# Kernel optimization log

Hardware: AMD Instinct MI355X
Metric: run time of the kernel (lower is better)

## Reference

```python
import jax, jax.numpy as jnp
from jax import lax
import numpy as np

K_IN, K_OUT, H, ML = 32, 16, 256, 80
L_PRE, L_FWD, B = 60, 80, 1024


def gru_cell(x, h, Wih, Whh, bih, bhh):
    # torch GRU gate order: r, z, n
    gi = x @ Wih.T + bih
    gh = h @ Whh.T + bhh
    ir, iz, inn = jnp.split(gi, 3, axis=-1)
    hr, hz, hn = jnp.split(gh, 3, axis=-1)
    r = jax.nn.sigmoid(ir + hr)
    z = jax.nn.sigmoid(iz + hz)
    n = jnp.tanh(inn + r * hn)
    return (1.0 - z) * n + z * h


def setup_inputs() -> dict:
    key = jax.random.key(0)
    ks = jax.random.split(key, 24)
    s = 0.05
    rn = lambda k, shp: (jax.random.normal(k, shp) * s).astype(jnp.float32)
    inp = {
        "pre_x": jax.random.normal(ks[0], (L_PRE, B, K_IN), dtype=jnp.float32),
        "pre_y": jax.random.normal(ks[1], (L_PRE, B, K_OUT), dtype=jnp.float32),
        "forward_x": jax.random.normal(ks[2], (L_FWD, B, K_IN), dtype=jnp.float32),
        # encoder: embedding Linear(k_in+k_out -> H), GRU(H,H)
        "enc_emb_W": rn(ks[3], (H, K_IN + K_OUT)),
        "enc_emb_b": rn(ks[4], (H,)),
        "enc_Wih": rn(ks[5], (3 * H, H)),
        "enc_Whh": rn(ks[6], (3 * H, H)),
        "enc_bih": rn(ks[7], (3 * H,)),
        "enc_bhh": rn(ks[8], (3 * H,)),
        # decoder: embedding Linear(k_out+k_in -> H), attn Linear(2H -> ML),
        # attn_combine Linear(2H -> H), GRU(H,H), out Linear(H -> k_out)
        "dec_emb_W": rn(ks[9], (H, K_OUT + K_IN)),
        "dec_emb_b": rn(ks[10], (H,)),
        "attn_W": rn(ks[11], (ML, 2 * H)),
        "attn_b": rn(ks[12], (ML,)),
        "comb_W": rn(ks[13], (H, 2 * H)),
        "comb_b": rn(ks[14], (H,)),
        "dec_Wih": rn(ks[15], (3 * H, H)),
        "dec_Whh": rn(ks[16], (3 * H, H)),
        "dec_bih": rn(ks[17], (3 * H,)),
        "dec_bhh": rn(ks[18], (3 * H,)),
        "out_W": rn(ks[19], (K_OUT, H)),
        "out_b": rn(ks[20], (K_OUT,)),
    }
    return inp


def reference(pre_x, pre_y, forward_x,
              enc_emb_W, enc_emb_b, enc_Wih, enc_Whh, enc_bih, enc_bhh,
              dec_emb_W, dec_emb_b, attn_W, attn_b, comb_W, comb_b,
              dec_Wih, dec_Whh, dec_bih, dec_bhh, out_W, out_b):
    L_pre, batch, _ = pre_x.shape
    hdim = enc_emb_b.shape[0]
    max_len = attn_b.shape[0]

    # ---- encoder ----
    emb = jnp.concatenate([pre_x, pre_y], axis=2) @ enc_emb_W.T + enc_emb_b  # [L_pre,B,H]
    h0 = jnp.zeros((batch, hdim), dtype=pre_x.dtype)

    def enc_step(h, x):
        h2 = gru_cell(x, h, enc_Wih, enc_Whh, enc_bih, enc_bhh)
        return h2, h2

    enc_h, enc_outs = lax.scan(enc_step, h0, emb)
    # pad encoder outputs to max_length along time (zeros beyond L_pre)
    enc_outputs = jnp.zeros((max_len, batch, hdim), dtype=pre_x.dtype).at[:L_pre].set(enc_outs)
    enc_bmh = enc_outputs.transpose(1, 0, 2)  # [B, ML, H]

    # ---- decoder (dropout inactive: eval mode) ----
    def dec_step(carry, fx):
        y, h = carry
        di = jnp.concatenate([y, fx], axis=-1)            # [B, k_out+k_in]
        e = di @ dec_emb_W.T + dec_emb_b                   # [B, H]
        logits = jnp.concatenate([e, h], axis=-1) @ attn_W.T + attn_b  # [B, ML]
        aw = jax.nn.softmax(logits, axis=-1)
        ctx = jnp.einsum('bm,bmh->bh', aw, enc_bmh)        # [B, H]
        g = jnp.tanh(jnp.concatenate([e, ctx], axis=-1) @ comb_W.T + comb_b)
        h2 = gru_cell(g, h, dec_Wih, dec_Whh, dec_bih, dec_bhh)
        y2 = h2 @ out_W.T + out_b                          # [B, k_out]
        return (y2, h2), y2

    y_init = jnp.zeros_like(pre_y[0])
    _, ys = lax.scan(dec_step, (y_init, enc_h), forward_x)
    return ys  # [L_fwd, B, k_out]
```

## Files before the change

kernel.cpp:

```cpp
#include <hip/hip_runtime.h>
#include <hip/hip_bf16.h>

#define BATCH 1024
#define HD 256
#define MLEN 80
#define LPRE 60
#define LFWD 80
#define KIN 32
#define KOUT 16

typedef unsigned short bf16_t;
typedef __attribute__((ext_vector_type(8))) short bf16x8;
typedef __attribute__((ext_vector_type(4))) float f32x4;
typedef __attribute__((ext_vector_type(4))) unsigned u32x4;

#define MFMA __builtin_amdgcn_mfma_f32_16x16x32_bf16

__device__ __forceinline__ float bf2f(bf16_t v){ return __uint_as_float(((unsigned)v)<<16); }
__device__ __forceinline__ bf16_t f2bf(float f){
    unsigned u = __float_as_uint(f);
    return (bf16_t)((u + 0x7FFFu + ((u>>16)&1u)) >> 16);
}
__device__ __forceinline__ unsigned pack2(float lo, float hi){
    return (unsigned)f2bf(lo) | ((unsigned)f2bf(hi)<<16);
}
__device__ __forceinline__ float bflo(unsigned d){ return __uint_as_float(d<<16); }
__device__ __forceinline__ float bfhi(unsigned d){ return __uint_as_float(d & 0xffff0000u); }
__device__ __forceinline__ float sigm(float x){ return 1.0f/(1.0f+__expf(-x)); }

#define OFF_Z  262144
#define OFF_IN 524288
#define OFF_HN 655360

__global__ void pack_gru(const float* __restrict__ Wih, const float* __restrict__ Whh,
                         bf16_t* __restrict__ dst)
{
    int T = blockIdx.x*256 + threadIdx.x;
    int grp, local;
    if (T < 16384){ grp=0; local=T; }
    else if (T < 32768){ grp=1; local=T-16384; }
    else if (T < 40960){ grp=2; local=T-32768; }
    else { grp=3; local=T-40960; }
    int nkt = (grp<2)?16:8;
    int nt  = local / (nkt*64);
    int rem = local - nt*(nkt*64);
    int kt  = rem >> 6;
    int l   = rem & 63;
    int n   = nt*16 + (l&15);
    int k0  = kt*32 + ((l>>4)<<3);
    unsigned w[4];
    #pragma unroll
    for (int h2=0; h2<4; h2++){
        float v[2];
        #pragma unroll
        for (int s=0; s<2; s++){
            int k = k0 + h2*2 + s;
            if (grp==0)      v[s] = (k<256)? Wih[(size_t)n*HD + k]       : Whh[(size_t)n*HD + (k-256)];
            else if (grp==1) v[s] = (k<256)? Wih[(size_t)(256+n)*HD + k] : Whh[(size_t)(256+n)*HD + (k-256)];
            else if (grp==2) v[s] = Wih[(size_t)(512+n)*HD + k];
            else             v[s] = Whh[(size_t)(512+n)*HD + k];
        }
        w[h2] = pack2(v[0], v[1]);
    }
    uint4 u = {w[0],w[1],w[2],w[3]};
    *(uint4*)((char*)dst + (size_t)T*16) = u;
}

__global__ void pack_B512(const float* __restrict__ W, bf16_t* __restrict__ dst)
{
    int T = blockIdx.x*256 + threadIdx.x;
    int nt = T >> 10, kt = (T>>6)&15, l = T&63;
    int n = nt*16 + (l&15);
    int k0 = kt*32 + ((l>>4)<<3);
    unsigned w[4];
    #pragma unroll
    for (int h2=0; h2<4; h2++)
        w[h2] = pack2(W[(size_t)n*512 + k0+h2*2], W[(size_t)n*512 + k0+h2*2+1]);
    uint4 u = {w[0],w[1],w[2],w[3]};
    *(uint4*)((char*)dst + (size_t)T*16) = u;
}

__global__ void wfuse_kernel(const float* __restrict__ dembW, const float* __restrict__ dembB,
                             const float* __restrict__ outW, const float* __restrict__ outB,
                             float* __restrict__ Wfuse, float* __restrict__ ebias)
{
    int T = blockIdx.x*256 + threadIdx.x;
    if (T < 65536){
        int k = T >> 8, n = T & 255;
        float acc = 0.f;
        #pragma unroll
        for (int o=0;o<16;o++) acc += dembW[(size_t)n*48 + o]*outW[(size_t)o*HD + k];
        Wfuse[(size_t)k*HD + n] = acc;
    } else if (T < 65792){
        int n = T - 65536;
        float acc = dembB[n];
        #pragma unroll
        for (int o=0;o<16;o++) acc += outB[o]*dembW[(size_t)n*48 + o];
        ebias[n] = acc;
    }
}

__global__ void pack_e(const float* __restrict__ Wfuse, const float* __restrict__ dembW,
                       bf16_t* __restrict__ dst)
{
    int T = blockIdx.x*256 + threadIdx.x;
    int nt = T/576, rem = T - nt*576;
    int kt = rem >> 6, l = rem & 63;
    int n = nt*16 + (l&15);
    int k0 = kt*32 + ((l>>4)<<3);
    unsigned w[4];
    #pragma unroll
    for (int h2=0; h2<4; h2++){
        float v[2];
        #pragma unroll
        for (int s=0;s<2;s++){
            int k = k0 + h2*2 + s;
            v[s] = (kt<8)? Wfuse[(size_t)k*HD + n] : dembW[(size_t)n*48 + 16 + (k-256)];
        }
        w[h2] = pack2(v[0], v[1]);
    }
    uint4 u = {w[0],w[1],w[2],w[3]};
    *(uint4*)((char*)dst + (size_t)T*16) = u;
}

__global__ void pack_logits(const float* __restrict__ Wfuse, const float* __restrict__ dembW,
                            const float* __restrict__ attW, const float* __restrict__ attB,
                            const float* __restrict__ dembB, const float* __restrict__ ebias,
                            bf16_t* __restrict__ BL, bf16_t* __restrict__ BL0,
                            float* __restrict__ lb, float* __restrict__ lb0)
{
    int T = blockIdx.x*256 + threadIdx.x;
    if (T < 5760){
        int variant = (T < 2880) ? 0 : 1;
        int local = variant ? (T-2880) : T;
        int nt = local/576, rem = local - nt*576;
        int kt = rem >> 6, l = rem & 63;
        int m  = nt*16 + (l&15);
        int k0 = kt*32 + ((l>>4)<<3);
        unsigned w[4];
        #pragma unroll
        for (int h2=0; h2<4; h2++){
            float v[2];
            for (int s=0;s<2;s++){
                int k = k0 + h2*2 + s;
                float acc;
                if (kt < 8){
                    if (variant == 0){
                        acc = attW[(size_t)m*512 + 256 + k];
                        for (int n=0;n<256;n++) acc += Wfuse[(size_t)k*HD + n]*attW[(size_t)m*512 + n];
                    } else {
                        acc = attW[(size_t)m*512 + 256 + k];
                    }
                } else {
                    int kp = k - 256;
                    acc = 0.f;
                    for (int n=0;n<256;n++) acc += dembW[(size_t)n*48 + 16 + kp]*attW[(size_t)m*512 + n];
                }
                v[s] = acc;
            }
            w[h2] = pack2(v[0], v[1]);
        }
        uint4 u = {w[0],w[1],w[2],w[3]};
        bf16_t* d = variant ? BL0 : BL;
        *(uint4*)((char*)d + (size_t)local*16) = u;
    } else if (T < 5840){
        int m = T - 5760;
        float acc = attB[m];
        for (int n=0;n<256;n++) acc += ebias[n]*attW[(size_t)m*512 + n];
        lb[m] = acc;
    } else if (T < 5920){
        int m = T - 5840;
        float acc = attB[m];
        for (int n=0;n<256;n++) acc += dembB[n]*attW[(size_t)m*512 + n];
        lb0[m] = acc;
    }
}

__global__ void pack_out(const float* __restrict__ outW, bf16_t* __restrict__ dst)
{
    int T = blockIdx.x*256 + threadIdx.x;
    int kt = T >> 6, l = T & 63;
    int n  = l & 15;
    int k0 = kt*32 + ((l>>4)<<3);
    unsigned w[4];
    #pragma unroll
    for (int h2=0; h2<4; h2++)
        w[h2] = pack2(outW[(size_t)n*HD + k0+h2*2], outW[(size_t)n*HD + k0+h2*2+1]);
    uint4 u = {w[0],w[1],w[2],w[3]};
    *(uint4*)((char*)dst + (size_t)T*16) = u;
}

__global__ __launch_bounds__(256) void emb_kernel(
    const float* __restrict__ px, const float* __restrict__ py,
    const float* __restrict__ embW, const float* __restrict__ embB,
    bf16_t* __restrict__ emb)
{
    __shared__ float Ws[256*49];
    __shared__ float xy[16][48];
    __shared__ float bs[256];
    int t = blockIdx.y, b0 = blockIdx.x*16, tid = threadIdx.x;
    for (int i = tid; i < 256*48; i += 256){ int n=i/48, k=i-n*48; Ws[n*49+k]=embW[i]; }
    bs[tid] = embB[tid];
    for (int i = tid; i < 16*48; i += 256){
        int r=i/48, k=i-r*48;
        xy[r][k] = (k<KIN)? px[((size_t)t*BATCH + b0+r)*KIN + k]
                          : py[((size_t)t*BATCH + b0+r)*KOUT + (k-KIN)];
    }
    __syncthreads();
    int n = tid;
    const float* w = &Ws[n*49];
    for (int r=0;r<16;r++){
        float acc = bs[n];
        #pragma unroll
        for (int k=0;k<48;k++) acc += xy[r][k]*w[k];
        emb[((size_t)t*BATCH + b0+r)*HD + n] = f2bf(acc);
    }
}

__global__ void fxconv(const float* __restrict__ fx, bf16_t* __restrict__ dst)
{
    size_t i = (size_t)blockIdx.x*256 + threadIdx.x;
    const float4* s = (const float4*)(fx + i*8);
    float4 a = s[0], b = s[1];
    uint4 u = { pack2(a.x,a.y), pack2(a.z,a.w), pack2(b.x,b.y), pack2(b.z,b.w) };
    *(uint4*)(dst + i*8) = u;
}

__global__ __launch_bounds__(512) void gru_step2(
    const bf16_t* __restrict__ A0, const bf16_t* __restrict__ A1,
    const bf16_t* __restrict__ Bp,
    const float* __restrict__ bih, const float* __restrict__ bhh,
    const float* __restrict__ hprev, float* __restrict__ hnext,
    bf16_t* __restrict__ hnext_bf, bf16_t* __restrict__ extra_bf)
{
    __shared__ __align__(16) bf16_t As[16][520];
    __shared__ __align__(16) f32x4 redR[4][64];
    __shared__ __align__(16) f32x4 redZ[4][64];
    __shared__ __align__(16) f32x4 redI[4][64];
    int tid = threadIdx.x, b0 = blockIdx.x*16;
    for (int i = tid; i < 1024; i += 512){
        int r = i>>6, c = i&63;
        const bf16_t* src = (c<32)? (A0 + (size_t)(b0+r)*HD + c*8)
                                  : (A1 + (size_t)(b0+r)*HD + (c-32)*8);
        *(uint4*)&As[r][c*8] = *(const uint4*)src;
    }
    __syncthreads();
    int lane = tid & 63, wave = tid >> 6;
    int pairId = wave >> 1, half = wave & 1;
    int jt = blockIdx.y*4 + pairId;
    const char* arow = (const char*)&As[lane&15][(lane>>4)*8];
    const char* bpc = (const char*)Bp;
    size_t loff = (size_t)lane*16;
    size_t offX = half ? (size_t)OFF_HN : (size_t)OFF_IN;
    int kt0 = half*8;
    f32x4 cr={0,0,0,0}, cz={0,0,0,0}, cx={0,0,0,0};
    #pragma unroll
    for (int k8=0; k8<8; k8++){
        int kt = kt0 + k8;
        bf16x8 a  = *(const bf16x8*)(arow + kt*64);
        bf16x8 br = *(const bf16x8*)(bpc + (size_t)(((jt<<4)+kt)<<10) + loff);
        bf16x8 bz = *(const bf16x8*)(bpc + OFF_Z + (size_t)(((jt<<4)+kt)<<10) + loff);
        bf16x8 bx = *(const bf16x8*)(bpc + offX + (size_t)(((jt<<3)+k8)<<10) + loff);
        cr = MFMA(a, br, cr, 0,0,0);
        cz = MFMA(a, bz, cz, 0,0,0);
        cx = MFMA(a, bx, cx, 0,0,0);
    }
    if (half == 0){
        redR[pairId][lane] = cr;
        redZ[pairId][lane] = cz;
        redI[pairId][lane] = cx;
    }
    __syncthreads();
    if (half == 1){
        f32x4 crA = redR[pairId][lane];
        f32x4 czA = redZ[pairId][lane];
        f32x4 ci  = redI[pairId][lane];
        int j = (jt<<4) + (lane&15);
        float b_r = bih[j] + bhh[j];
        float b_z = bih[256+j] + bhh[256+j];
        float b_i = bih[512+j], b_h = bhh[512+j];
        #pragma unroll
        for (int q=0;q<4;q++){
            int b = b0 + ((lane>>4)<<2) + q;
            float rv = sigm(cr[q] + crA[q] + b_r);
            float zv = sigm(cz[q] + czA[q] + b_z);
            float nv = tanhf(ci[q] + b_i + rv*(cx[q] + b_h));
            float h2 = (1.0f - zv)*nv + zv*hprev[(size_t)b*HD + j];
            hnext[(size_t)b*HD + j] = h2;
            bf16_t hb = f2bf(h2);
            hnext_bf[(size_t)b*HD + j] = hb;
            extra_bf[(size_t)b*HD + j] = hb;
        }
    }
}

__global__ __launch_bounds__(1024) void dec_front(
    const bf16_t* __restrict__ hbf, const bf16_t* __restrict__ fxt,
    const bf16_t* __restrict__ enc_out,
    const bf16_t* __restrict__ Be, const bf16_t* __restrict__ BL,
    const bf16_t* __restrict__ Bcmb, const bf16_t* __restrict__ Bout,
    const float* __restrict__ ebp, const float* __restrict__ lbp,
    const float* __restrict__ combB, const float* __restrict__ outB,
    int t, bf16_t* __restrict__ g_out, float* __restrict__ out)
{
    __shared__ __align__(16) bf16_t As[16][296];
    __shared__ __align__(16) bf16_t Eb[16][264];
    __shared__ __align__(16) bf16_t Cb[16][264];
    __shared__ float awL[16][84];
    __shared__ float Cpart[16][256];

    int tid = threadIdx.x, b0 = blockIdx.x*16;

    if (tid < 576){
        int r = tid/36, c = tid - r*36;
        const bf16_t* src = (c<32)? (hbf + (size_t)(b0+r)*HD + c*8)
                                  : (fxt + (size_t)(b0+r)*KIN + (c-32)*8);
        *(uint4*)&As[r][c*8] = *(const uint4*)src;
    }

    int half = tid >> 9;
    int u    = tid & 511;
    int cr_  = u >> 5;
    int cc0  = (u & 31) * 8;
    const bf16_t* cbp = enc_out + ((size_t)(half*30)*BATCH + (b0+cr_))*HD + cc0;
    u32x4 pf[10];
    #pragma unroll
    for (int i=0;i<10;i++) pf[i] = *(const u32x4*)(cbp + (size_t)i*BATCH*HD);

    __syncthreads();

    int lane = tid & 63, wave = tid >> 6;
    const bf16_t* arow = &As[lane&15][(lane>>4)*8];
    size_t loff = (size_t)lane*16;
    int ke0 = t ? 0 : 8;

    {
        f32x4 c = {0,0,0,0};
        for (int kt = ke0; kt < 9; kt++){
            bf16x8 a = *(const bf16x8*)(arow + kt*32);
            bf16x8 b = *(const bf16x8*)((const char*)Be + (size_t)((wave*9+kt)<<10) + loff);
            c = MFMA(a, b, c, 0,0,0);
        }
        int n = (wave<<4) + (lane&15);
        float bbn = ebp[n];
        #pragma unroll
        for (int q=0;q<4;q++) Eb[((lane>>4)<<2)+q][n] = f2bf(c[q] + bbn);
    }
    if (wave < 5){
        f32x4 c = {0,0,0,0};
        #pragma unroll
        for (int kt = 0; kt < 9; kt++){
            bf16x8 a = *(const bf16x8*)(arow + kt*32);
            bf16x8 b = *(const bf16x8*)((const char*)BL + (size_t)((wave*9+kt)<<10) + loff);
            c = MFMA(a, b, c, 0,0,0);
        }
        int m = (wave<<4) + (lane&15);
        float bbm = lbp[m];
        #pragma unroll
        for (int q=0;q<4;q++) awL[((lane>>4)<<2)+q][m] = c[q] + bbm;
    } else if (wave == 5 && t > 0){
        f32x4 c = {0,0,0,0};
        #pragma unroll
        for (int kt = 0; kt < 8; kt++){
            bf16x8 a = *(const bf16x8*)(arow + kt*32);
            bf16x8 b = *(const bf16x8*)((const char*)Bout + (size_t)(kt<<10) + loff);
            c = MFMA(a, b, c, 0,0,0);
        }
        int o = lane & 15;
        float bo = outB[o];
        #pragma unroll
        for (int q=0;q<4;q++){
            int r = ((lane>>4)<<2) + q;
            out[((size_t)(t-1)*BATCH + b0+r)*KOUT + o] = c[q] + bo;
        }
    }
    __syncthreads();

    if (tid < 256){
        int r2 = tid >> 4, l2 = tid & 15;
        float vmax = -1e30f;
        for (int m=l2; m<80; m+=16) vmax = fmaxf(vmax, awL[r2][m]);
        #pragma unroll
        for (int k=1; k<16; k<<=1) vmax = fmaxf(vmax, __shfl_xor(vmax, k, 16));
        float ps = 0.f;
        for (int m=l2; m<80; m+=16){ float v = __expf(awL[r2][m]-vmax); awL[r2][m]=v; ps += v; }
        #pragma unroll
        for (int k=1; k<16; k<<=1) ps += __shfl_xor(ps, k, 16);
        float inv = 1.0f/ps;
        for (int m=l2; m<80; m+=16) awL[r2][m] *= inv;
    }
    __syncthreads();

    float acc[8];
    #pragma unroll
    for (int i=0;i<8;i++) acc[i] = 0.f;
    {
        const float* awr = &awL[cr_][half*30];
        #pragma unroll
        for (int i=0;i<10;i++){
            float w = awr[i];
            acc[0] = fmaf(w, bflo(pf[i][0]), acc[0]);
            acc[1] = fmaf(w, bfhi(pf[i][0]), acc[1]);
            acc[2] = fmaf(w, bflo(pf[i][1]), acc[2]);
            acc[3] = fmaf(w, bfhi(pf[i][1]), acc[3]);
            acc[4] = fmaf(w, bflo(pf[i][2]), acc[4]);
            acc[5] = fmaf(w, bfhi(pf[i][2]), acc[5]);
            acc[6] = fmaf(w, bflo(pf[i][3]), acc[6]);
            acc[7] = fmaf(w, bfhi(pf[i][3]), acc[7]);
        }
        #pragma unroll 5
        for (int i=10;i<30;i++){
            u32x4 v = *(const u32x4*)(cbp + (size_t)i*BATCH*HD);
            float w = awr[i];
            acc[0] = fmaf(w, bflo(v[0]), acc[0]);
            acc[1] = fmaf(w, bfhi(v[0]), acc[1]);
            acc[2] = fmaf(w, bflo(v[1]), acc[2]);
            acc[3] = fmaf(w, bfhi(v[1]), acc[3]);
            acc[4] = fmaf(w, bflo(v[2]), acc[4]);
            acc[5] = fmaf(w, bfhi(v[2]), acc[5]);
            acc[6] = fmaf(w, bflo(v[3]), acc[6]);
            acc[7] = fmaf(w, bfhi(v[3]), acc[7]);
        }
    }
    if (half == 0){
        float4 p0 = {acc[0],acc[1],acc[2],acc[3]};
        float4 p1 = {acc[4],acc[5],acc[6],acc[7]};
        *(float4*)&Cpart[cr_][cc0]   = p0;
        *(float4*)&Cpart[cr_][cc0+4] = p1;
    }
    __syncthreads();

    if (half == 1){
        float4 p0 = *(const float4*)&Cpart[cr_][cc0];
        float4 p1 = *(const float4*)&Cpart[cr_][cc0+4];
        uint4 ov;
        ov.x = pack2(acc[0]+p0.x, acc[1]+p0.y);
        ov.y = pack2(acc[2]+p0.z, acc[3]+p0.w);
        ov.z = pack2(acc[4]+p1.x, acc[5]+p1.y);
        ov.w = pack2(acc[6]+p1.z, acc[7]+p1.w);
        *(uint4*)&Cb[cr_][cc0] = ov;
    }
    __syncthreads();

    {
        const bf16_t* ae = &Eb[lane&15][(lane>>4)*8];
        const bf16_t* ac = &Cb[lane&15][(lane>>4)*8];
        f32x4 c = {0,0,0,0};
        #pragma unroll
        for (int kt=0; kt<16; kt++){
            bf16x8 a = (kt<8)? *(const bf16x8*)(ae + kt*32)
                             : *(const bf16x8*)(ac + (kt-8)*32);
            bf16x8 b = *(const bf16x8*)((const char*)Bcmb + (size_t)(((wave<<4)+kt)<<10) + loff);
            c = MFMA(a, b, c, 0,0,0);
        }
        int n = (wave<<4) + (lane&15);
        float bbn = combB[n];
        #pragma unroll
        for (int q=0;q<4;q++){
            int r = ((lane>>4)<<2) + q;
            g_out[(size_t)(b0+r)*HD + n] = f2bf(tanhf(c[q] + bbn));
        }
    }
}

__global__ __launch_bounds__(256) void final79(
    const float* __restrict__ hf, const float* __restrict__ outW,
    const float* __restrict__ outB, float* __restrict__ ys)
{
    __shared__ float hs[16][260];
    __shared__ float ow[16*260];
    int tid = threadIdx.x, b0 = blockIdx.x*16;
    for (int i=tid;i<4096;i+=256){ int o2=i>>8,k=i&255; ow[o2*260+k]=outW[(size_t)o2*HD+k]; }
    for (int i=tid;i<4096;i+=256){ int r=i>>8,k=i&255; hs[r][k]=hf[(size_t)(b0+r)*HD+k]; }
    __syncthreads();
    int r=tid>>4, o=tid&15;
    float acc=outB[o];
    const float* w=&ow[o*260];
    for(int k=0;k<256;k++) acc += hs[r][k]*w[k];
    ys[((size_t)79*BATCH + b0+r)*KOUT + o] = acc;
}

extern "C" void kernel_launch(void* const* d_in, const int* in_sizes, int n_in,
                              void* d_out, int out_size, void* d_ws, size_t ws_size,
                              hipStream_t stream) {
    const float* pre_x    = (const float*)d_in[0];
    const float* pre_y    = (const float*)d_in[1];
    const float* fwd_x    = (const float*)d_in[2];
    const float* enc_embW = (const float*)d_in[3];
    const float* enc_embB = (const float*)d_in[4];
    const float* enc_Wih  = (const float*)d_in[5];
    const float* enc_Whh  = (const float*)d_in[6];
    const float* enc_bih  = (const float*)d_in[7];
    const float* enc_bhh  = (const float*)d_in[8];
    const float* dec_embW = (const float*)d_in[9];
    const float* dec_embB = (const float*)d_in[10];
    const float* attn_W   = (const float*)d_in[11];
    const float* attn_b   = (const float*)d_in[12];
    const float* comb_W   = (const float*)d_in[13];
    const float* comb_b   = (const float*)d_in[14];
    const float* dec_Wih  = (const float*)d_in[15];
    const float* dec_Whh  = (const float*)d_in[16];
    const float* dec_bih  = (const float*)d_in[17];
    const float* dec_bhh  = (const float*)d_in[18];
    const float* out_W    = (const float*)d_in[19];
    const float* out_b    = (const float*)d_in[20];
    float* out = (float*)d_out;

    char* ws = (char*)d_ws;
    size_t o = 0;
    auto alloc = [&](size_t bytes)->char*{
        char* p = ws + o; o = (o + bytes + 255) & ~(size_t)255; return p;
    };
    bf16_t* EMB     = (bf16_t*)alloc((size_t)LPRE*BATCH*HD*2);
    bf16_t* ENC_OUT = (bf16_t*)alloc((size_t)LPRE*BATCH*HD*2);
    bf16_t* FXB     = (bf16_t*)alloc((size_t)LFWD*BATCH*KIN*2);
    float*  HF0     = (float*) alloc((size_t)BATCH*HD*4);
    float*  HF1     = (float*) alloc((size_t)BATCH*HD*4);
    bf16_t* HB0     = (bf16_t*)alloc((size_t)BATCH*HD*2);
    bf16_t* HB1     = (bf16_t*)alloc((size_t)BATCH*HD*2);
    bf16_t* GBUF    = (bf16_t*)alloc((size_t)BATCH*HD*2);
    bf16_t* DUMMY   = (bf16_t*)alloc((size_t)BATCH*HD*2);
    float*  WFUSE   = (float*) alloc((size_t)256*256*4);
    float*  EBIAS   = (float*) alloc(256*4);
    float*  LB      = (float*) alloc(80*4);
    float*  LB0     = (float*) alloc(80*4);
    bf16_t* PACK_ENC = (bf16_t*)alloc(786432);
    bf16_t* PACK_DEC = (bf16_t*)alloc(786432);
    bf16_t* PACK_CMB = (bf16_t*)alloc(262144);
    bf16_t* PACK_E   = (bf16_t*)alloc(147456);
    bf16_t* PACK_BL  = (bf16_t*)alloc(46080);
    bf16_t* PACK_BL0 = (bf16_t*)alloc(46080);
    bf16_t* PACK_OUT = (bf16_t*)alloc(8192);

    hipMemsetAsync(HF0, 0, (size_t)BATCH*HD*4, stream);
    hipMemsetAsync(HB0, 0, (size_t)BATCH*HD*2, stream);

    dim3 blk(256);
    emb_kernel<<<dim3(64,60), blk, 0, stream>>>(pre_x, pre_y, enc_embW, enc_embB, EMB);
    fxconv<<<dim3(1280), blk, 0, stream>>>(fwd_x, FXB);
    pack_gru<<<dim3(192), blk, 0, stream>>>(enc_Wih, enc_Whh, PACK_ENC);
    pack_gru<<<dim3(192), blk, 0, stream>>>(dec_Wih, dec_Whh, PACK_DEC);
    pack_B512<<<dim3(64), blk, 0, stream>>>(comb_W, PACK_CMB);
    wfuse_kernel<<<dim3(257), blk, 0, stream>>>(dec_embW, dec_embB, out_W, out_b, WFUSE, EBIAS);
    pack_e<<<dim3(36), blk, 0, stream>>>(WFUSE, dec_embW, PACK_E);
    pack_logits<<<dim3(24), blk, 0, stream>>>(WFUSE, dec_embW, attn_W, attn_b, dec_embB,
                                              EBIAS, PACK_BL, PACK_BL0, LB, LB0);
    pack_out<<<dim3(2), blk, 0, stream>>>(out_W, PACK_OUT);

    float*  HF[2] = {HF0, HF1};
    bf16_t* HB[2] = {HB0, HB1};
    int p = 0;

    for (int t = 0; t < LPRE; t++){
        gru_step2<<<dim3(64,4), dim3(512), 0, stream>>>(
            EMB + (size_t)t*BATCH*HD, HB[p], PACK_ENC, enc_bih, enc_bhh,
            HF[p], HF[p^1], HB[p^1], ENC_OUT + (size_t)t*BATCH*HD);
        p ^= 1;
    }
    for (int t = 0; t < LFWD; t++){
        const bf16_t* fxt = FXB + (size_t)t*BATCH*KIN;
        dec_front<<<dim3(64), dim3(1024), 0, stream>>>(
            HB[p], fxt, ENC_OUT,
            PACK_E, t ? PACK_BL : PACK_BL0, PACK_CMB, PACK_OUT,
            t ? EBIAS : dec_embB, t ? LB : LB0, comb_b, out_b,
            t, GBUF, out);
        gru_step2<<<dim3(64,4), dim3(512), 0, stream>>>(
            GBUF, HB[p], PACK_DEC, dec_bih, dec_bhh,
            HF[p], HF[p^1], HB[p^1], DUMMY);
        p ^= 1;
    }
    final79<<<dim3(64), blk, 0, stream>>>(HF[p], out_W, out_b, out);
}
```

Before: 2.462 ms.

## Fold combine weights into embedding and precompute encoder-side combine projection

Precomputes P = enc_out @ comb_W[:,256:]^T once after the encoder, so the context term of attn_combine becomes a weighted sum of projected rows. It also folds the decoder embedding weights into comb_W, so g comes from one GEMM on [h, fx] plus the attention-weighted P. The decoder front is split into an attention/softmax kernel and a 4-way column-parallel combine kernel, giving 256 blocks instead of 64 for the combine step. The cost is an extra kernel launch per step, the attention weights round-tripping through global memory, and extra bf16 rounding in P.

```diff
diff --git a/kernel.cpp b/kernel.cpp
--- a/kernel.cpp
+++ b/kernel.cpp
@@ -98,29 +98,6 @@
         for (int o=0;o<16;o++) acc += outB[o]*dembW[(size_t)n*48 + o];
         ebias[n] = acc;
     }
-}
-
-__global__ void pack_e(const float* __restrict__ Wfuse, const float* __restrict__ dembW,
-                       bf16_t* __restrict__ dst)
-{
-    int T = blockIdx.x*256 + threadIdx.x;
-    int nt = T/576, rem = T - nt*576;
-    int kt = rem >> 6, l = rem & 63;
-    int n = nt*16 + (l&15);
-    int k0 = kt*32 + ((l>>4)<<3);
-    unsigned w[4];
-    #pragma unroll
-    for (int h2=0; h2<4; h2++){
-        float v[2];
-        #pragma unroll
-        for (int s=0;s<2;s++){
-            int k = k0 + h2*2 + s;
-            v[s] = (kt<8)? Wfuse[(size_t)k*HD + n] : dembW[(size_t)n*48 + 16 + (k-256)];
-        }
-        w[h2] = pack2(v[0], v[1]);
-    }
-    uint4 u = {w[0],w[1],w[2],w[3]};
-    *(uint4*)((char*)dst + (size_t)T*16) = u;
 }
 
 __global__ void pack_logits(const float* __restrict__ Wfuse, const float* __restrict__ dembW,
@@ -176,6 +153,48 @@
     }
 }
 
+__global__ void pack_gfold(const float* __restrict__ Wfuse, const float* __restrict__ dembW,
+                           const float* __restrict__ combW, const float* __restrict__ combB,
+                           const float* __restrict__ ebias, const float* __restrict__ dembB,
+                           bf16_t* __restrict__ dst, float* __restrict__ cbf, float* __restrict__ cbf0)
+{
+    int T = blockIdx.x*256 + threadIdx.x;
+    if (T < 9216){
+        int nt = T/576, rem = T - nt*576;
+        int kt = rem >> 6, l = rem & 63;
+        int n = nt*16 + (l&15);
+        int k0 = kt*32 + ((l>>4)<<3);
+        unsigned w[4];
+        for (int h2=0; h2<4; h2++){
+            float v[2];
+            for (int s=0;s<2;s++){
+                int k = k0 + h2*2 + s;
+                float acc = 0.f;
+                if (k < 256){
+                    for (int j=0;j<256;j++) acc += Wfuse[(size_t)k*HD + j]*combW[(size_t)n*512 + j];
+                } else {
+                    int kp = k - 256;
+                    for (int j=0;j<256;j++) acc += dembW[(size_t)j*48 + 16 + kp]*combW[(size_t)n*512 + j];
+                }
+                v[s] = acc;
+            }
+            w[h2] = pack2(v[0], v[1]);
+        }
+        uint4 u = {w[0],w[1],w[2],w[3]};
+        *(uint4*)((char*)dst + (size_t)T*16) = u;
+    } else if (T < 9472){
+        int n = T - 9216;
+        float acc = combB[n];
+        for (int j=0;j<256;j++) acc += ebias[j]*combW[(size_t)n*512 + j];
+        cbf[n] = acc;
+    } else if (T < 9728){
+        int n = T - 9472;
+        float acc = combB[n];
+        for (int j=0;j<256;j++) acc += dembB[j]*combW[(size_t)n*512 + j];
+        cbf0[n] = acc;
+    }
+}
+
 __global__ void pack_out(const float* __restrict__ outW, bf16_t* __restrict__ dst)
 {
     int T = blockIdx.x*256 + threadIdx.x;
@@ -226,6 +245,44 @@
     *(uint4*)(dst + i*8) = u;
 }
 
+__global__ __launch_bounds__(256) void pgemm(
+    const bf16_t* __restrict__ enc, const bf16_t* __restrict__ Bcmb,
+    bf16_t* __restrict__ P)
+{
+    __shared__ __align__(16) bf16_t As[16][264];
+    __shared__ __align__(16) bf16_t Gs[16][264];
+    int tid = threadIdx.x, b0 = blockIdx.x*16, t = blockIdx.y;
+    const bf16_t* src = enc + ((size_t)t*BATCH + b0)*HD;
+    for (int i = tid; i < 512; i += 256){
+        int r = i>>5, c = i&31;
+        *(uint4*)&As[r][c*8] = *(const uint4*)(src + (size_t)r*HD + c*8);
+    }
+    __syncthreads();
+    int lane = tid&63, wave = tid>>6;
+    const bf16_t* arow = &As[lane&15][(lane>>4)*8];
+    size_t loff = (size_t)lane*16;
+    #pragma unroll
+    for (int u=0; u<4; u++){
+        int nt = wave*4 + u;
+        f32x4 c = {0,0,0,0};
+        #pragma unroll
+        for (int k8=0; k8<8; k8++){
+            bf16x8 a = *(const bf16x8*)(arow + k8*32);
+            bf16x8 b = *(const bf16x8*)((const char*)Bcmb + (size_t)(((nt<<4)+8+k8)<<10) + loff);
+            c = MFMA(a, b, c, 0,0,0);
+        }
+        int n = (nt<<4) + (lane&15);
+        #pragma unroll
+        for (int q=0;q<4;q++) Gs[((lane>>4)<<2)+q][n] = f2bf(c[q]);
+    }
+    __syncthreads();
+    bf16_t* dst = P + ((size_t)t*BATCH + b0)*HD;
+    for (int i = tid; i < 512; i += 256){
+        int r = i>>5, c = i&31;
+        *(uint4*)(dst + (size_t)r*HD + c*8) = *(const uint4*)&Gs[r][c*8];
+    }
+}
+
 __global__ __launch_bounds__(512) void gru_step2(
     const bf16_t* __restrict__ A0, const bf16_t* __restrict__ A1,
     const bf16_t* __restrict__ Bp,
@@ -294,58 +351,25 @@
     }
 }
 
-__global__ __launch_bounds__(1024) void dec_front(
+__global__ __launch_bounds__(512) void dec_attn(
     const bf16_t* __restrict__ hbf, const bf16_t* __restrict__ fxt,
-    const bf16_t* __restrict__ enc_out,
-    const bf16_t* __restrict__ Be, const bf16_t* __restrict__ BL,
-    const bf16_t* __restrict__ Bcmb, const bf16_t* __restrict__ Bout,
-    const float* __restrict__ ebp, const float* __restrict__ lbp,
-    const float* __restrict__ combB, const float* __restrict__ outB,
-    int t, bf16_t* __restrict__ g_out, float* __restrict__ out)
+    const bf16_t* __restrict__ BL, const bf16_t* __restrict__ Bout,
+    const float* __restrict__ lbp, const float* __restrict__ outB,
+    int t, float* __restrict__ aw, float* __restrict__ out)
 {
     __shared__ __align__(16) bf16_t As[16][296];
-    __shared__ __align__(16) bf16_t Eb[16][264];
-    __shared__ __align__(16) bf16_t Cb[16][264];
     __shared__ float awL[16][84];
-    __shared__ float Cpart[16][256];
-
     int tid = threadIdx.x, b0 = blockIdx.x*16;
-
-    if (tid < 576){
-        int r = tid/36, c = tid - r*36;
+    for (int i = tid; i < 576; i += 512){
+        int r = i/36, c = i - r*36;
         const bf16_t* src = (c<32)? (hbf + (size_t)(b0+r)*HD + c*8)
                                   : (fxt + (size_t)(b0+r)*KIN + (c-32)*8);
         *(uint4*)&As[r][c*8] = *(const uint4*)src;
     }
-
-    int half = tid >> 9;
-    int u    = tid & 511;
-    int cr_  = u >> 5;
-    int cc0  = (u & 31) * 8;
-    const bf16_t* cbp = enc_out + ((size_t)(half*30)*BATCH + (b0+cr_))*HD + cc0;
-    u32x4 pf[10];
-    #pragma unroll
-    for (int i=0;i<10;i++) pf[i] = *(const u32x4*)(cbp + (size_t)i*BATCH*HD);
-
-    __syncthreads();
-
+    __syncthreads();
     int lane = tid & 63, wave = tid >> 6;
     const bf16_t* arow = &As[lane&15][(lane>>4)*8];
     size_t loff = (size_t)lane*16;
-    int ke0 = t ? 0 : 8;
-
-    {
-        f32x4 c = {0,0,0,0};
-        for (int kt = ke0; kt < 9; kt++){
-            bf16x8 a = *(const bf16x8*)(arow + kt*32);
-            bf16x8 b = *(const bf16x8*)((const char*)Be + (size_t)((wave*9+kt)<<10) + loff);
-            c = MFMA(a, b, c, 0,0,0);
-        }
-        int n = (wave<<4) + (lane&15);
-        float bbn = ebp[n];
-        #pragma unroll
-        for (int q=0;q<4;q++) Eb[((lane>>4)<<2)+q][n] = f2bf(c[q] + bbn);
-    }
     if (wave < 5){
         f32x4 c = {0,0,0,0};
         #pragma unroll
@@ -375,7 +399,6 @@
         }
     }
     __syncthreads();
-
     if (tid < 256){
         int r2 = tid >> 4, l2 = tid & 15;
         float vmax = -1e30f;
@@ -387,79 +410,99 @@
         #pragma unroll
         for (int k=1; k<16; k<<=1) ps += __shfl_xor(ps, k, 16);
         float inv = 1.0f/ps;
-        for (int m=l2; m<80; m+=16) awL[r2][m] *= inv;
-    }
-    __syncthreads();
+        for (int m=l2; m<80; m+=16) aw[(size_t)(b0+r2)*80 + m] = awL[r2][m]*inv;
+    }
+}
+
+__global__ __launch_bounds__(256) void dec_gcomb(
+    const bf16_t* __restrict__ hbf, const bf16_t* __restrict__ fxt,
+    const float* __restrict__ aw, const bf16_t* __restrict__ P,
+    const bf16_t* __restrict__ Bgf, const float* __restrict__ cbf,
+    int kt0, bf16_t* __restrict__ g_out)
+{
+    __shared__ __align__(16) bf16_t As[16][296];
+    __shared__ float aws[16][80];
+    __shared__ float pre[16][68];
+    __shared__ float part[2][16][64];
+    int tid = threadIdx.x, b0 = blockIdx.x*16, y = blockIdx.y;
+
+    int half = tid >> 7;
+    int u = tid & 127;
+    int r_ = u >> 3;
+    int c8 = u & 7;
+    const bf16_t* pbp = P + ((size_t)(half*30)*BATCH + (b0+r_))*HD + y*64 + c8*8;
+    u32x4 pf[15];
+    #pragma unroll
+    for (int i=0;i<15;i++) pf[i] = *(const u32x4*)(pbp + (size_t)i*BATCH*HD);
+
+    for (int i = tid; i < 576; i += 256){
+        int r = i/36, c = i - r*36;
+        const bf16_t* src = (c<32)? (hbf + (size_t)(b0+r)*HD + c*8)
+                                  : (fxt + (size_t)(b0+r)*KIN + (c-32)*8);
+        *(uint4*)&As[r][c*8] = *(const uint4*)src;
+    }
+    for (int i = tid; i < 1280; i += 256){
+        int r = i/80, m = i - r*80;
+        aws[r][m] = aw[(size_t)(b0+r)*80 + m];
+    }
+    __syncthreads();
+
+    int lane = tid & 63, wave = tid >> 6;
+    {
+        const bf16_t* arow = &As[lane&15][(lane>>4)*8];
+        size_t loff = (size_t)lane*16;
+        int nt = y*4 + wave;
+        f32x4 c = {0,0,0,0};
+        for (int kt=kt0; kt<9; kt++){
+            bf16x8 a = *(const bf16x8*)(arow + kt*32);
+            bf16x8 b = *(const bf16x8*)((const char*)Bgf + (size_t)((nt*9+kt)<<10) + loff);
+            c = MFMA(a, b, c, 0,0,0);
+        }
+        #pragma unroll
+        for (int q=0;q<4;q++) pre[((lane>>4)<<2)+q][wave*16 + (lane&15)] = c[q];
+    }
 
     float acc[8];
     #pragma unroll
-    for (int i=0;i<8;i++) acc[i] = 0.f;
+    for (int i=0;i<8;i++) acc[i]=0.f;
+    const float* awr = &aws[r_][half*30];
+    #pragma unroll
+    for (int i=0;i<15;i++){
+        float w = awr[i];
+        acc[0]=fmaf(w,bflo(pf[i][0]),acc[0]); acc[1]=fmaf(w,bfhi(pf[i][0]),acc[1]);
+        acc[2]=fmaf(w,bflo(pf[i][1]),acc[2]); acc[3]=fmaf(w,bfhi(pf[i][1]),acc[3]);
+        acc[4]=fmaf(w,bflo(pf[i][2]),acc[4]); acc[5]=fmaf(w,bfhi(pf[i][2]),acc[5]);
+        acc[6]=fmaf(w,bflo(pf[i][3]),acc[6]); acc[7]=fmaf(w,bfhi(pf[i][3]),acc[7]);
+    }
+    #pragma unroll 5
+    for (int i=15;i<30;i++){
+        u32x4 v = *(const u32x4*)(pbp + (size_t)i*BATCH*HD);
+        float w = awr[i];
+        acc[0]=fmaf(w,bflo(v[0]),acc[0]); acc[1]=fmaf(w,bfhi(v[0]),acc[1]);
+        acc[2]=fmaf(w,bflo(v[1]),acc[2]); acc[3]=fmaf(w,bfhi(v[1]),acc[3]);
+        acc[4]=fmaf(w,bflo(v[2]),acc[4]); acc[5]=fmaf(w,bfhi(v[2]),acc[5]);
+        acc[6]=fmaf(w,bflo(v[3]),acc[6]); acc[7]=fmaf(w,bfhi(v[3]),acc[7]);
+    }
     {
-        const float* awr = &awL[cr_][half*30];
-        #pragma unroll
-        for (int i=0;i<10;i++){
-            float w = awr[i];
-            acc[0] = fmaf(w, bflo(pf[i][0]), acc[0]);
-            acc[1] = fmaf(w, bfhi(pf[i][0]), acc[1]);
-            acc[2] = fmaf(w, bflo(pf[i][1]), acc[2]);
-            acc[3] = fmaf(w, bfhi(pf[i][1]), acc[3]);
-            acc[4] = fmaf(w, bflo(pf[i][2]), acc[4]);
-            acc[5] = fmaf(w, bfhi(pf[i][2]), acc[5]);
-            acc[6] = fmaf(w, bflo(pf[i][3]), acc[6]);
-            acc[7] = fmaf(w, bfhi(pf[i][3]), acc[7]);
-        }
-        #pragma unroll 5
-        for (int i=10;i<30;i++){
-            u32x4 v = *(const u32x4*)(cbp + (size_t)i*BATCH*HD);
-            float w = awr[i];
-            acc[0] = fmaf(w, bflo(v[0]), acc[0]);
-            acc[1] = fmaf(w, bfhi(v[0]), acc[1]);
-            acc[2] = fmaf(w, bflo(v[1]), acc[2]);
-            acc[3] = fmaf(w, bfhi(v[1]), acc[3]);
-            acc[4] = fmaf(w, bflo(v[2]), acc[4]);
-            acc[5] = fmaf(w, bfhi(v[2]), acc[5]);
-            acc[6] = fmaf(w, bflo(v[3]), acc[6]);
-            acc[7] = fmaf(w, bfhi(v[3]), acc[7]);
-        }
-    }
-    if (half == 0){
         float4 p0 = {acc[0],acc[1],acc[2],acc[3]};
         float4 p1 = {acc[4],acc[5],acc[6],acc[7]};
-        *(float4*)&Cpart[cr_][cc0]   = p0;
-        *(float4*)&Cpart[cr_][cc0+4] = p1;
-    }
-    __syncthreads();
-
-    if (half == 1){
-        float4 p0 = *(const float4*)&Cpart[cr_][cc0];
-        float4 p1 = *(const float4*)&Cpart[cr_][cc0+4];
-        uint4 ov;
-        ov.x = pack2(acc[0]+p0.x, acc[1]+p0.y);
-        ov.y = pack2(acc[2]+p0.z, acc[3]+p0.w);
-        ov.z = pack2(acc[4]+p1.x, acc[5]+p1.y);
-        ov.w = pack2(acc[6]+p1.z, acc[7]+p1.w);
-        *(uint4*)&Cb[cr_][cc0] = ov;
-    }
-    __syncthreads();
-
-    {
-        const bf16_t* ae = &Eb[lane&15][(lane>>4)*8];
-        const bf16_t* ac = &Cb[lane&15][(lane>>4)*8];
-        f32x4 c = {0,0,0,0};
-        #pragma unroll
-        for (int kt=0; kt<16; kt++){
-            bf16x8 a = (kt<8)? *(const bf16x8*)(ae + kt*32)
-                             : *(const bf16x8*)(ac + (kt-8)*32);
-            bf16x8 b = *(const bf16x8*)((const char*)Bcmb + (size_t)(((wave<<4)+kt)<<10) + loff);
-            c = MFMA(a, b, c, 0,0,0);
-        }
-        int n = (wave<<4) + (lane&15);
-        float bbn = combB[n];
-        #pragma unroll
-        for (int q=0;q<4;q++){
-            int r = ((lane>>4)<<2) + q;
-            g_out[(size_t)(b0+r)*HD + n] = f2bf(tanhf(c[q] + bbn));
-        }
+        *(float4*)&part[half][r_][c8*8]   = p0;
+        *(float4*)&part[half][r_][c8*8+4] = p1;
+    }
+    __syncthreads();
+
+    if (tid < 128){
+        int r = tid >> 3, cc = (tid & 7)*8;
+        int n0 = y*64 + cc;
+        unsigned ov[4];
+        #pragma unroll
+        for (int p2=0;p2<4;p2++){
+            float g0 = tanhf(pre[r][cc+p2*2]   + part[0][r][cc+p2*2]   + part[1][r][cc+p2*2]   + cbf[n0+p2*2]);
+            float g1 = tanhf(pre[r][cc+p2*2+1] + part[0][r][cc+p2*2+1] + part[1][r][cc+p2*2+1] + cbf[n0+p2*2+1]);
+            ov[p2] = pack2(g0, g1);
+        }
+        uint4 uu = {ov[0],ov[1],ov[2],ov[3]};
+        *(uint4*)(g_out + (size_t)(b0+r)*HD + n0) = uu;
     }
 }
 
@@ -513,6 +556,7 @@
     };
     bf16_t* EMB     = (bf16_t*)alloc((size_t)LPRE*BATCH*HD*2);
     bf16_t* ENC_OUT = (bf16_t*)alloc((size_t)LPRE*BATCH*HD*2);
+    bf16_t* PBUF    = (bf16_t*)alloc((size_t)LPRE*BATCH*HD*2);
     bf16_t* FXB     = (bf16_t*)alloc((size_t)LFWD*BATCH*KIN*2);
     float*  HF0     = (float*) alloc((size_t)BATCH*HD*4);
     float*  HF1     = (float*) alloc((size_t)BATCH*HD*4);
@@ -520,14 +564,17 @@
     bf16_t* HB1     = (bf16_t*)alloc((size_t)BATCH*HD*2);
     bf16_t* GBUF    = (bf16_t*)alloc((size_t)BATCH*HD*2);
     bf16_t* DUMMY   = (bf16_t*)alloc((size_t)BATCH*HD*2);
+    float*  AWB     = (float*) alloc((size_t)BATCH*80*4);
     float*  WFUSE   = (float*) alloc((size_t)256*256*4);
     float*  EBIAS   = (float*) alloc(256*4);
     float*  LB      = (float*) alloc(80*4);
     float*  LB0     = (float*) alloc(80*4);
+    float*  CBF     = (float*) alloc(256*4);
+    float*  CBF0    = (float*) alloc(256*4);
     bf16_t* PACK_ENC = (bf16_t*)alloc(786432);
     bf16_t* PACK_DEC = (bf16_t*)alloc(786432);
     bf16_t* PACK_CMB = (bf16_t*)alloc(262144);
-    bf16_t* PACK_E   = (bf16_t*)alloc(147456);
+    bf16_t* PACK_GF  = (bf16_t*)alloc(147456);
     bf16_t* PACK_BL  = (bf16_t*)alloc(46080);
     bf16_t* PACK_BL0 = (bf16_t*)alloc(46080);
     bf16_t* PACK_OUT = (bf16_t*)alloc(8192);
@@ -542,9 +589,10 @@
     pack_gru<<<dim3(192), blk, 0, stream>>>(dec_Wih, dec_Whh, PACK_DEC);
     pack_B512<<<dim3(64), blk, 0, stream>>>(comb_W, PACK_CMB);
     wfuse_kernel<<<dim3(257), blk, 0, stream>>>(dec_embW, dec_embB, out_W, out_b, WFUSE, EBIAS);
-    pack_e<<<dim3(36), blk, 0, stream>>>(WFUSE, dec_embW, PACK_E);
     pack_logits<<<dim3(24), blk, 0, stream>>>(WFUSE, dec_embW, attn_W, attn_b, dec_embB,
                                               EBIAS, PACK_BL, PACK_BL0, LB, LB0);
+    pack_gfold<<<dim3(38), blk, 0, stream>>>(WFUSE, dec_embW, comb_W, comb_b,
+                                             EBIAS, dec_embB, PACK_GF, CBF, CBF0);
     pack_out<<<dim3(2), blk, 0, stream>>>(out_W, PACK_OUT);
 
     float*  HF[2] = {HF0, HF1};
@@ -557,13 +605,15 @@
             HF[p], HF[p^1], HB[p^1], ENC_OUT + (size_t)t*BATCH*HD);
         p ^= 1;
     }
+    pgemm<<<dim3(64,60), blk, 0, stream>>>(ENC_OUT, PACK_CMB, PBUF);
+
     for (int t = 0; t < LFWD; t++){
         const bf16_t* fxt = FXB + (size_t)t*BATCH*KIN;
-        dec_front<<<dim3(64), dim3(1024), 0, stream>>>(
-            HB[p], fxt, ENC_OUT,
-            PACK_E, t ? PACK_BL : PACK_BL0, PACK_CMB, PACK_OUT,
-            t ? EBIAS : dec_embB, t ? LB : LB0, comb_b, out_b,
-            t, GBUF, out);
+        dec_attn<<<dim3(64), dim3(512), 0, stream>>>(
+            HB[p], fxt, t ? PACK_BL : PACK_BL0, PACK_OUT,
+            t ? LB : LB0, out_b, t, AWB, out);
+        dec_gcomb<<<dim3(64,4), blk, 0, stream>>>(
+            HB[p], fxt, AWB, PBUF, PACK_GF, t ? CBF : CBF0, t ? 0 : 8, GBUF);
         gru_step2<<<dim3(64,4), dim3(512), 0, stream>>>(
             GBUF, HB[p], PACK_DEC, dec_bih, dec_bhh,
             HF[p], HF[p^1], HB[p^1], DUMMY);
```

Result: slower. 2.553 ms (+3.7%).
